# Kernel tuning notes

Hardware: AMD Instinct MI355X
Metric: run time of the kernel (lower is better)

## Reference

```python
import jax, jax.numpy as jnp
import numpy as np

T, L, H, C, D_IN, ED, N, E = 4, 3, 1, 256, 20, 10, 4096, 65536
D = H * C  # 256, pooling width
AH = 4     # pooling attention heads


def setup_inputs() -> dict:
    key = jax.random.key(0)
    ks = jax.random.split(key, 24)
    g = lambda k, s, sc=0.05: jax.random.normal(k, s, jnp.float32) * sc
    return {
        "x": jax.random.normal(ks[0], (N, D_IN), jnp.float32),
        "src": jax.random.randint(ks[1], (E,), 0, N),
        "dst": jax.random.randint(ks[2], (E,), 0, N),
        "edge_attr": jax.random.normal(ks[3], (E, ED), jnp.float32),
        "edge_type": jax.random.randint(ks[4], (E,), 0, T),
        # GATConv params per (edge_type, layer)
        "W0": g(ks[5], (T, D_IN, H * C)),          # layer 0 lin
        "W12": g(ks[6], (T, 2, H * C, H * C)),     # layers 1,2 lin
        "att_src": g(ks[7], (T, L, H, C)),
        "att_dst": g(ks[8], (T, L, H, C)),
        "att_edge": g(ks[9], (T, L, H, C)),
        "lin_edge_w": g(ks[10], (T, L, ED, H * C)),
        "biases": g(ks[11], (T, L, C)),            # H=1 so concat/mean both give C
        "edge_type_weights": jnp.ones((T,), jnp.float32) / T,
        # pooling: MultiheadAttention(D, 4 heads)
        "in_proj_w": g(ks[12], (3 * D, D)),
        "in_proj_b": g(ks[13], (3 * D,)),
        "out_proj_w": g(ks[14], (D, D)),
        "out_proj_b": g(ks[15], (D,)),
        # fusion MLP: 3D -> 2D -> 256
        "fus_w1": g(ks[16], (3 * D, 2 * D)),
        "fus_b1": g(ks[17], (2 * D,)),
        "fus_w2": g(ks[18], (2 * D, 256)),
        "fus_b2": g(ks[19], (256,)),
    }


def _gat(h, src, dst, mask, e_attr, W, a_s, a_d, a_e, We, b, concat):
    # PyG GATConv (edge_dim, add_self_loops=True, fill_value='mean'), eval mode
    Nn = h.shape[0]
    Hh, Cc = a_s.shape
    xl = (h @ W).reshape(Nn, Hh, Cc)
    s_src = jnp.sum(xl * a_s, -1)   # [N,H]
    s_dst = jnp.sum(xl * a_d, -1)   # [N,H]
    s_e = jnp.sum((e_attr @ We).reshape(-1, Hh, Cc) * a_e, -1)  # [E,H]
    # self-loop edge_attr = per-node mean of masked incoming edge_attr
    m = mask.astype(h.dtype)
    cnt = jax.ops.segment_sum(m, dst, Nn)
    loop_attr = jax.ops.segment_sum(e_attr * m[:, None], dst, Nn) / jnp.maximum(cnt, 1.0)[:, None]
    s_loop = jnp.sum((loop_attr @ We).reshape(Nn, Hh, Cc) * a_e, -1)  # [N,H]
    a_real = jax.nn.leaky_relu(s_src[src] + s_dst[dst] + s_e, 0.2)
    a_real = jnp.where(mask[:, None], a_real, -1e30)  # mask edges not of this type
    a_loop = jax.nn.leaky_relu(s_src + s_dst + s_loop, 0.2)
    ar = jnp.arange(Nn)
    idx = jnp.concatenate([dst, ar])    # destination of each (edge + self-loop)
    sidx = jnp.concatenate([src, ar])   # source of each
    scores = jnp.concatenate([a_real, a_loop], 0)  # [E+N, H]
    smax = jax.ops.segment_max(scores, idx, Nn)
    ex = jnp.exp(scores - smax[idx])
    ssum = jax.ops.segment_sum(ex, idx, Nn)
    alpha = ex / (ssum[idx] + 1e-16)
    out = jax.ops.segment_sum(xl[sidx] * alpha[:, :, None], idx, Nn)  # [N,H,C]
    out = out.reshape(Nn, Hh * Cc) if concat else out.mean(1)
    return out + b


def reference(x, src, dst, edge_attr, edge_type, W0, W12, att_src, att_dst,
              att_edge, lin_edge_w, biases, edge_type_weights, in_proj_w,
              in_proj_b, out_proj_w, out_proj_b, fus_w1, fus_b1, fus_w2, fus_b2):
    outs = []
    for t in range(T):
        mask = edge_type == t
        h = x
        for i in range(L):
            W = W0[t] if i == 0 else W12[t, i - 1]
            h = _gat(h, src, dst, mask, edge_attr, W, att_src[t, i],
                     att_dst[t, i], att_edge[t, i], lin_edge_w[t, i],
                     biases[t, i], concat=(i < L - 1))
            h = jax.nn.elu(h)  # dropout off in eval
        outs.append(h)
    w = jax.nn.softmax(edge_type_weights)
    h = sum(w[t] * outs[t] for t in range(T))  # [N, D]
    # HierarchicalGraphPooling
    mean_p = h.mean(0)
    max_p = h.max(0)
    qkv = h @ in_proj_w.T + in_proj_b
    q, k, v = jnp.split(qkv, 3, axis=-1)
    HD = D // AH
    q = q.reshape(-1, AH, HD)
    k = k.reshape(-1, AH, HD)
    v = v.reshape(-1, AH, HD)
    att = jax.nn.softmax(jnp.einsum('nhd,mhd->hnm', q, k) / np.float32(np.sqrt(HD)), axis=-1)
    o = jnp.einsum('hnm,mhd->nhd', att, v).reshape(-1, D) @ out_proj_w.T + out_proj_b
    attn_p = o.mean(0)
    comb = jnp.concatenate([mean_p, max_p, attn_p])  # [3D]
    g = jax.nn.relu(comb @ fus_w1 + fus_b1)
    g = jax.nn.relu(g @ fus_w2 + fus_b2)
    return g[None, :]
```

## Files before the change

### kernel.cpp

```cpp
#include <hip/hip_runtime.h>
#include <math.h>

#define T 4
#define LL 3
#define C 256
#define DIN 20
#define NN 4096
#define EE 65536
#define AHD 4
#define MCH 8
#define QKS 72
#define AST 264
#define SLOTN (16384*64)

#define W_CURSOR 0
#define W_SLSRC  16384
#define F_SLSE   (W_SLSRC + SLOTN)
#define F_XL     (F_SLSE + 3*SLOTN)
#define F_H      (F_XL + T*NN*C/2)
#define F_OPART  F_XL
#define F_SSRC   (F_H + T*NN*C/2)
#define F_SDST   (F_SSRC + T*NN)
#define F_WE     (F_SDST + T*NN)
#define F_HACC   (F_WE + 128)
#define F_WT     (F_HACC + NN*C/2)
#define F_QKV    (F_WT + 768*256/2)
#define F_DPART  (F_QKV + NN*768/2)
#define F_MEANP  (F_DPART + MCH*NN*AHD)
#define F_MAXP   (F_MEANP + C)
#define F_OMEAN  (F_MAXP + C)
#define F_PART   (F_OMEAN + C)
#define U_W12P   (F_PART + 16*512)
#define WS_WORDS (U_W12P + 262144)

static __device__ __forceinline__ float lrelu(float x){ return x > 0.f ? x : 0.2f*x; }
static __device__ __forceinline__ float eluf(float x){ return x > 0.f ? x : __expf(x) - 1.f; }

typedef _Float16 half2_t __attribute__((ext_vector_type(2)));
typedef _Float16 v8h __attribute__((ext_vector_type(8)));
typedef float v4f __attribute__((ext_vector_type(4)));

static __device__ __forceinline__ unsigned pk2(float x, float y){
  half2_t h; h.x = (_Float16)x; h.y = (_Float16)y;
  return __builtin_bit_cast(unsigned, h);
}
static __device__ __forceinline__ unsigned pk2h(_Float16 x, _Float16 y){
  half2_t h; h.x = x; h.y = y;
  return __builtin_bit_cast(unsigned, h);
}
static __device__ __forceinline__ float4 up4(uint2 u){
  half2_t a = __builtin_bit_cast(half2_t, u.x);
  half2_t b = __builtin_bit_cast(half2_t, u.y);
  return make_float4((float)a.x, (float)a.y, (float)b.x, (float)b.y);
}
static __device__ __forceinline__ uint2 dn4(float4 v){
  return make_uint2(pk2(v.x, v.y), pk2(v.z, v.w));
}

static __device__ inline void atomicMaxF(float* addr, float val){
  int* ai = (int*)addr;
  int old = __float_as_int(*addr);
  while (__int_as_float(old) < val){
    int assumed = old;
    old = atomicCAS(ai, assumed, __float_as_int(val));
    if (old == assumed) break;
  }
}

__global__ __launch_bounds__(256) void prep_k(
    const float* __restrict__ x, const float* __restrict__ W0,
    const float* __restrict__ attS, const float* __restrict__ attD,
    _Float16* __restrict__ xlo, float* __restrict__ ssrc, float* __restrict__ sdst,
    const float* __restrict__ w12, _Float16* __restrict__ wpT,
    const float* __restrict__ ipw, _Float16* __restrict__ ip16,
    const float* __restrict__ linE, const float* __restrict__ attE,
    float* we, float* fbase, int* cursor){
  __shared__ float smem[64*65];
  __shared__ float red[64];
  int by = blockIdx.y, bx = blockIdx.x, tid = threadIdx.x;
  if (by < 4){
    int t = by;
    const float* W = W0 + (size_t)t*DIN*C;
    int n0 = bx*8;
    for (int j = 0; j < 8; j++)
      for (int k = tid; k < DIN; k += 256)
        smem[j*DIN + k] = x[(n0+j)*DIN + k];
    __syncthreads();
    float acc[8] = {0,0,0,0,0,0,0,0};
    int c = tid;
    for (int k = 0; k < DIN; k += 4){
      float w0 = W[(k+0)*C + c], w1 = W[(k+1)*C + c], w2 = W[(k+2)*C + c], w3 = W[(k+3)*C + c];
      #pragma unroll
      for (int j = 0; j < 8; j++){
        float4 h4 = *(const float4*)&smem[j*DIN + k];
        acc[j] += w0*h4.x + w1*h4.y + w2*h4.z + w3*h4.w;
      }
    }
    #pragma unroll
    for (int j = 0; j < 8; j++) xlo[((size_t)t*NN + n0 + j)*C + c] = (_Float16)acc[j];
    float aS = attS[t*LL*C + c], aD = attD[t*LL*C + c];
    int lane = c & 63, w = c >> 6;
    #pragma unroll
    for (int j = 0; j < 8; j++){
      float v1 = acc[j]*aS, v2 = acc[j]*aD;
      #pragma unroll
      for (int off = 32; off > 0; off >>= 1){ v1 += __shfl_down(v1, off); v2 += __shfl_down(v2, off); }
      if (lane == 0){ red[j*8 + w] = v1; red[j*8 + 4 + w] = v2; }
    }
    __syncthreads();
    if (c < 16){
      int j = c >> 1, which = c & 1;
      const float* r = red + j*8 + which*4;
      float s = r[0] + r[1] + r[2] + r[3];
      (which ? sdst : ssrc)[t*NN + n0 + j] = s;
    }
  } else if (by < 12){
    if (bx < 16){
      int b8 = by - 4;
      int k0 = (bx >> 2)*64, n0 = (bx & 3)*64;
      const float* src = w12 + ((size_t)b8*256 + k0)*256 + n0;
      int row = tid >> 2, l4 = (tid & 3)*4;
      #pragma unroll
      for (int pass = 0; pass < 4; pass++){
        float4 v = *(const float4*)(src + (size_t)row*256 + pass*16 + l4);
        int o = row*65 + pass*16 + l4;
        smem[o+0] = v.x; smem[o+1] = v.y; smem[o+2] = v.z; smem[o+3] = v.w;
      }
      __syncthreads();
      int n = tid >> 2, seg = tid & 3;
      _Float16* dstp = wpT + ((size_t)b8*256 + n0 + n)*256 + k0 + seg*16;
      v8h h0, h1;
      #pragma unroll
      for (int i = 0; i < 8; i++) h0[i] = (_Float16)smem[(seg*16 + i)*65 + n];
      #pragma unroll
      for (int i = 0; i < 8; i++) h1[i] = (_Float16)smem[(seg*16 + 8 + i)*65 + n];
      *(v8h*)(dstp) = h0;
      *(v8h*)(dstp + 8) = h1;
    }
  } else if (by < 15){
    if (bx < 256){
      int j = (by - 12)*256 + bx;
      ip16[(size_t)j*256 + tid] = (_Float16)ipw[(size_t)j*256 + tid];
    }
  } else {
    if (bx < 12){
      int t = bx / 3, l = bx % 3;
      float ae = attE[(t*LL + l)*C + tid];
      const float* lw = linE + (size_t)((t*LL + l)*10)*C;
      for (int k = 0; k < 10; k++) smem[k*C + tid] = lw[k*C + tid]*ae;
      __syncthreads();
      if (tid < 10){
        float s = 0.f;
        for (int i = 0; i < C; i++) s += smem[tid*C + i];
        we[(t*LL + l)*10 + tid] = s;
      }
    } else if (bx == 12){
      fbase[tid] = 0.f;
      fbase[256 + tid] = -1e30f;
      fbase[512 + tid] = 0.f;
    } else if (bx >= 64 && bx < 128){
      cursor[(bx - 64)*256 + tid] = 0;
    }
  }
}

__global__ __launch_bounds__(256) void scat_k(const int* __restrict__ dst, const int* __restrict__ ety,
                                              const int* __restrict__ srcv, const float* __restrict__ eattr,
                                              const float* __restrict__ we,
                                              int* cursor, int* slot_src, float* slot_se){
  int e = blockIdx.x*256 + threadIdx.x;
  if (e < EE){
    int t = ety[e];
    int gid = dst[e]*T + t;
    int p = atomicAdd(&cursor[gid], 1);
    if (p < 64){
      int sl = gid*64 + p;
      slot_src[sl] = srcv[e];
      float ea[10];
      #pragma unroll
      for (int k = 0; k < 10; k++) ea[k] = eattr[(size_t)e*10 + k];
      #pragma unroll
      for (int l = 0; l < 3; l++){
        const float* w = we + (t*LL + l)*10;
        float s = 0.f;
        #pragma unroll
        for (int k = 0; k < 10; k++) s += ea[k]*w[k];
        slot_se[(size_t)l*SLOTN + sl] = s;
      }
    }
  }
}

__global__ __launch_bounds__(256, 2) void gemm16m_k(const _Float16* __restrict__ hin,
                                                    const _Float16* __restrict__ wpT,
                                                    const float* __restrict__ attS, const float* __restrict__ attD,
                                                    int l, _Float16* __restrict__ xlo,
                                                    float* __restrict__ ssrc, float* __restrict__ sdst){
  __shared__ __align__(16) _Float16 As[64*AST];
  __shared__ float redS[4*64], redD[4*64];
  int t = blockIdx.y;
  int mb = blockIdx.x*64;
  int tid = threadIdx.x;
  int w = tid >> 6, lane = tid & 63;
  int r16 = lane & 15, q = lane >> 4;
  {
    int sr = tid >> 2, sc = (tid & 3)*64;
    const _Float16* hr = hin + ((size_t)(t*NN + mb + sr))*C + sc;
    #pragma unroll
    for (int i = 0; i < 8; i++)
      *(v8h*)(As + (size_t)sr*AST + sc + 8*i) = *(const v8h*)(hr + 8*i);
  }
  __syncthreads();
  int cb = w*64;
  const _Float16* WB = wpT + ((size_t)((t*2 + (l-1))*256 + cb))*256;
  v4f o[4][4];
  #pragma unroll
  for (int i = 0; i < 4; i++)
    #pragma unroll
    for (int j = 0; j < 4; j++) o[i][j] = (v4f){0.f,0.f,0.f,0.f};
  #pragma unroll
  for (int kk = 0; kk < 8; kk++){
    v8h a[4], b[4];
    #pragma unroll
    for (int mi = 0; mi < 4; mi++) a[mi] = *(v8h*)(As + (size_t)(mi*16 + r16)*AST + kk*32 + q*8);
    #pragma unroll
    for (int ni = 0; ni < 4; ni++) b[ni] = *(const v8h*)(WB + (size_t)(ni*16 + r16)*256 + kk*32 + q*8);
    #pragma unroll
    for (int mi = 0; mi < 4; mi++)
      #pragma unroll
      for (int ni = 0; ni < 4; ni++)
        o[mi][ni] = __builtin_amdgcn_mfma_f32_16x16x32_f16(a[mi], b[ni], o[mi][ni], 0, 0, 0);
  }
  int tl = t*LL + l;
  float aS[4], aD[4];
  #pragma unroll
  for (int ni = 0; ni < 4; ni++){
    aS[ni] = attS[tl*C + cb + ni*16 + r16];
    aD[ni] = attD[tl*C + cb + ni*16 + r16];
  }
  #pragma unroll
  for (int mi = 0; mi < 4; mi++)
    #pragma unroll
    for (int rr = 0; rr < 4; rr++){
      int row = mb + mi*16 + q*4 + rr;
      float v1 = 0.f, v2 = 0.f;
      #pragma unroll
      for (int ni = 0; ni < 4; ni++){
        float ov = o[mi][ni][rr];
        xlo[((size_t)t*NN + row)*C + cb + ni*16 + r16] = (_Float16)ov;
        v1 += ov*aS[ni]; v2 += ov*aD[ni];
      }
      v1 += __shfl_xor(v1, 1); v2 += __shfl_xor(v2, 1);
      v1 += __shfl_xor(v1, 2); v2 += __shfl_xor(v2, 2);
      v1 += __shfl_xor(v1, 4); v2 += __shfl_xor(v2, 4);
      v1 += __shfl_xor(v1, 8); v2 += __shfl_xor(v2, 8);
      if (r16 == 0){
        redS[w*64 + mi*16 + q*4 + rr] = v1;
        redD[w*64 + mi*16 + q*4 + rr] = v2;
      }
    }
  __syncthreads();
  if (tid < 64)
    ssrc[t*NN + mb + tid] = redS[tid] + redS[64+tid] + redS[128+tid] + redS[192+tid];
  else if (tid < 128){
    int i = tid - 64;
    sdst[t*NN + mb + i] = redD[i] + redD[64+i] + redD[128+i] + redD[192+i];
  }
}

__global__ __launch_bounds__(256, 2) void qkv16m_k(const _Float16* __restrict__ hacc,
                                                   const _Float16* __restrict__ ip16,
                                                   const float* __restrict__ ipb, _Float16* __restrict__ qkv,
                                                   float* meanp, float* maxp){
  __shared__ __align__(16) _Float16 As[64*AST];
  int p = blockIdx.y;
  int mb = blockIdx.x*64;
  int tid = threadIdx.x;
  int w = tid >> 6, lane = tid & 63;
  int r16 = lane & 15, q = lane >> 4;
  {
    int sr = tid >> 2, sc = (tid & 3)*64;
    const _Float16* hr = hacc + ((size_t)(mb + sr))*C + sc;
    #pragma unroll
    for (int i = 0; i < 8; i++)
      *(v8h*)(As + (size_t)sr*AST + sc + 8*i) = *(const v8h*)(hr + 8*i);
  }
  __syncthreads();
  int cb = p*256 + w*64;
  v4f o[4][4];
  #pragma unroll
  for (int i = 0; i < 4; i++)
    #pragma unroll
    for (int j = 0; j < 4; j++) o[i][j] = (v4f){0.f,0.f,0.f,0.f};
  #pragma unroll
  for (int kk = 0; kk < 8; kk++){
    v8h a[4], b[4];
    #pragma unroll
    for (int mi = 0; mi < 4; mi++) a[mi] = *(v8h*)(As + (size_t)(mi*16 + r16)*AST + kk*32 + q*8);
    #pragma unroll
    for (int ni = 0; ni < 4; ni++) b[ni] = *(const v8h*)(ip16 + (size_t)(cb + ni*16 + r16)*256 + kk*32 + q*8);
    #pragma unroll
    for (int mi = 0; mi < 4; mi++)
      #pragma unroll
      for (int ni = 0; ni < 4; ni++)
        o[mi][ni] = __builtin_amdgcn_mfma_f32_16x16x32_f16(a[mi], b[ni], o[mi][ni], 0, 0, 0);
  }
  float bn[4];
  #pragma unroll
  for (int ni = 0; ni < 4; ni++) bn[ni] = ipb[cb + ni*16 + r16];
  #pragma unroll
  for (int mi = 0; mi < 4; mi++)
    #pragma unroll
    for (int rr = 0; rr < 4; rr++){
      int row = mb + mi*16 + q*4 + rr;
      #pragma unroll
      for (int ni = 0; ni < 4; ni++)
        qkv[(size_t)row*768 + cb + ni*16 + r16] = (_Float16)(o[mi][ni][rr] + bn[ni]);
    }
  if (p == 0){
    float sm = 0.f, mx = -1e30f;
    for (int r = 0; r < 64; r++){
      float v = (float)hacc[(size_t)(mb + r)*C + tid];
      sm += v; mx = fmaxf(mx, v);
    }
    atomicAdd(&meanp[tid], sm*(1.f/4096.f));
    atomicMaxF(&maxp[tid], mx);
  }
}

__global__ __launch_bounds__(256) void agg_k(const _Float16* __restrict__ xl, const float* __restrict__ ssrc,
                                             const float* __restrict__ sdst,
                                             const int* __restrict__ cnt, const int* __restrict__ slot_src,
                                             const float* __restrict__ slot_se,
                                             const float* __restrict__ bias, _Float16* __restrict__ hout,
                                             const float* __restrict__ etw, _Float16* __restrict__ hacc, int l){
  __shared__ float4 sh[4][64];
  int gid = blockIdx.x*4 + (threadIdx.x >> 6);
  int lane = threadIdx.x & 63;
  int n = gid >> 2, t = gid & 3;
  int deg = cnt[gid];
  if (deg > 64) deg = 64;
  float sd = sdst[t*NN + n];
  float se_e = 0.f; int sj = 0;
  if (lane < deg){
    int sl = gid*64 + lane;
    sj = slot_src[sl];
    se_e = slot_se[(size_t)l*SLOTN + sl];
  }
  float ssum_se = se_e;
  #pragma unroll
  for (int o = 32; o > 0; o >>= 1) ssum_se += __shfl_xor(ssum_se, o);
  float sloop = ssum_se / (float)(deg > 0 ? deg : 1);
  float sc = (lane < deg) ? lrelu(ssrc[t*NN + sj] + sd + se_e) : -1e30f;
  float al = lrelu(ssrc[t*NN + n] + sd + sloop);
  float mx = fmaxf(sc, al);
  #pragma unroll
  for (int o = 32; o > 0; o >>= 1) mx = fmaxf(mx, __shfl_xor(mx, o));
  float ex = (lane < deg) ? __expf(sc - mx) : 0.f;
  float ale = __expf(al - mx);
  float ssum = ex;
  #pragma unroll
  for (int o = 32; o > 0; o >>= 1) ssum += __shfl_xor(ssum, o);
  float inv = 1.f/(ssum + ale + 1e-16f);
  const uint2* xl2 = (const uint2*)xl;
  float4 acc = up4(xl2[((size_t)(t*NN + n))*64 + lane]);
  acc.x *= ale; acc.y *= ale; acc.z *= ale; acc.w *= ale;
  int dmax = deg - 1;
  for (int j0 = 0; j0 < deg; j0 += 4){
    float p0 = __shfl(ex, j0);
    float p1 = (j0+1 < deg) ? __shfl(ex, j0+1) : 0.f;
    float p2 = (j0+2 < deg) ? __shfl(ex, j0+2) : 0.f;
    float p3 = (j0+3 < deg) ? __shfl(ex, j0+3) : 0.f;
    int s0 = __shfl(sj, j0);
    int s1 = __shfl(sj, (j0+1 < deg) ? j0+1 : dmax);
    int s2 = __shfl(sj, (j0+2 < deg) ? j0+2 : dmax);
    int s3 = __shfl(sj, (j0+3 < deg) ? j0+3 : dmax);
    float4 v0 = up4(xl2[((size_t)(t*NN + s0))*64 + lane]);
    float4 v1 = up4(xl2[((size_t)(t*NN + s1))*64 + lane]);
    float4 v2 = up4(xl2[((size_t)(t*NN + s2))*64 + lane]);
    float4 v3 = up4(xl2[((size_t)(t*NN + s3))*64 + lane]);
    acc.x += p0*v0.x + p1*v1.x + p2*v2.x + p3*v3.x;
    acc.y += p0*v0.y + p1*v1.y + p2*v2.y + p3*v3.y;
    acc.z += p0*v0.z + p1*v1.z + p2*v2.z + p3*v3.z;
    acc.w += p0*v0.w + p1*v1.w + p2*v2.w + p3*v3.w;
  }
  float4 b4 = *(const float4*)&bias[(t*LL + l)*C + lane*4];
  acc.x = eluf(acc.x*inv + b4.x); acc.y = eluf(acc.y*inv + b4.y);
  acc.z = eluf(acc.z*inv + b4.z); acc.w = eluf(acc.w*inv + b4.w);
  if (l < 2){
    ((uint2*)hout)[((size_t)(t*NN + n))*64 + lane] = dn4(acc);
  } else {
    sh[t][lane] = acc;
    __syncthreads();
    if (t == 0){
      float e0 = etw[0], e1 = etw[1], e2 = etw[2], e3 = etw[3];
      float m = fmaxf(fmaxf(e0,e1), fmaxf(e2,e3));
      float w0 = __expf(e0-m), w1 = __expf(e1-m), w2 = __expf(e2-m), w3 = __expf(e3-m);
      float winv = 1.f/(w0+w1+w2+w3);
      float4 v0 = sh[0][lane], v1 = sh[1][lane], v2 = sh[2][lane], v3 = sh[3][lane];
      float4 s;
      s.x = (w0*v0.x + w1*v1.x + w2*v2.x + w3*v3.x)*winv;
      s.y = (w0*v0.y + w1*v1.y + w2*v2.y + w3*v3.y)*winv;
      s.z = (w0*v0.z + w1*v1.z + w2*v2.z + w3*v3.z)*winv;
      s.w = (w0*v0.w + w1*v1.w + w2*v2.w + w3*v3.w)*winv;
      ((uint2*)hacc)[(size_t)n*64 + lane] = dn4(s);
    }
  }
}

__global__ __launch_bounds__(256, 2) void attn_k(const _Float16* __restrict__ qkv,
                                                 _Float16* __restrict__ opart,
                                                 float* __restrict__ dpart){
  __shared__ __align__(16) _Float16 Ks[64*QKS];
  __shared__ __align__(16) _Float16 VTs[64*QKS];
  __shared__ __align__(16) _Float16 Ps[4][64*QKS];
  int tid = threadIdx.x;
  int wave = tid >> 6, l = tid & 63;
  int nb = blockIdx.x*256 + wave*64;
  int h = blockIdx.y, mc = blockIdx.z;
  int r16 = l & 15, q = l >> 4;
  _Float16* Pw = Ps[wave];

  v8h qf[4][2];
  #pragma unroll
  for (int ni = 0; ni < 4; ni++){
    const _Float16* qrow = qkv + (size_t)(nb + ni*16 + r16)*768 + h*64;
    #pragma unroll
    for (int kk = 0; kk < 2; kk++){
      v8h hv = *(const v8h*)(qrow + kk*32 + q*8);
      #pragma unroll
      for (int i = 0; i < 8; i++) hv[i] = hv[i] * (_Float16)0.125f;
      qf[ni][kk] = hv;
    }
  }

  v4f o[4][4];
  #pragma unroll
  for (int i = 0; i < 4; i++)
    #pragma unroll
    for (int j = 0; j < 4; j++) o[i][j] = (v4f){0.f,0.f,0.f,0.f};
  float dn[4] = {0.f,0.f,0.f,0.f};

  for (int mt = 0; mt < NN/MCH/64; mt++){
    int mb = mc*(NN/MCH) + mt*64;
    __syncthreads();
    {
      int sr = tid >> 2, sc = (tid & 3)*16;
      const _Float16* krow = qkv + (size_t)(mb + sr)*768 + 256 + h*64 + sc;
      *(v8h*)(Ks + (size_t)sr*QKS + sc) = *(const v8h*)(krow);
      *(v8h*)(Ks + (size_t)sr*QKS + sc + 8) = *(const v8h*)(krow + 8);
    }
    {
      int m0 = (tid & 31)*2;
      int db = (tid >> 5)*8;
      const _Float16* v0 = qkv + (size_t)(mb + m0)*768 + 512 + h*64 + db;
      const _Float16* v1 = v0 + 768;
      v8h a = *(const v8h*)v0;
      v8h b = *(const v8h*)v1;
      #pragma unroll
      for (int d = 0; d < 8; d++)
        *(unsigned*)(VTs + (size_t)(db+d)*QKS + m0) = pk2h(a[d], b[d]);
    }
    __syncthreads();
    v4f c[4][4];
    #pragma unroll
    for (int i = 0; i < 4; i++)
      #pragma unroll
      for (int j = 0; j < 4; j++) c[i][j] = (v4f){0.f,0.f,0.f,0.f};
    #pragma unroll
    for (int kk = 0; kk < 2; kk++){
      v8h a[4];
      #pragma unroll
      for (int mi = 0; mi < 4; mi++) a[mi] = *(v8h*)(Ks + (size_t)(mi*16 + r16)*QKS + kk*32 + q*8);
      #pragma unroll
      for (int mi = 0; mi < 4; mi++)
        #pragma unroll
        for (int ni = 0; ni < 4; ni++)
          c[mi][ni] = __builtin_amdgcn_mfma_f32_16x16x32_f16(a[mi], qf[ni][kk], c[mi][ni], 0, 0, 0);
    }
    #pragma unroll
    for (int mi = 0; mi < 4; mi++)
      #pragma unroll
      for (int ni = 0; ni < 4; ni++){
        float e0 = __expf(c[mi][ni][0]), e1 = __expf(c[mi][ni][1]),
              e2 = __expf(c[mi][ni][2]), e3 = __expf(c[mi][ni][3]);
        dn[ni] += e0 + e1 + e2 + e3;
        *(uint2*)(Pw + (size_t)(ni*16 + r16)*QKS + mi*16 + q*4) = make_uint2(pk2(e0,e1), pk2(e2,e3));
      }
    #pragma unroll
    for (int km = 0; km < 2; km++){
      v8h pa[4], vb[4];
      #pragma unroll
      for (int ni = 0; ni < 4; ni++) pa[ni] = *(v8h*)(Pw + (size_t)(ni*16 + r16)*QKS + km*32 + q*8);
      #pragma unroll
      for (int di = 0; di < 4; di++) vb[di] = *(v8h*)(VTs + (size_t)(di*16 + r16)*QKS + km*32 + q*8);
      #pragma unroll
      for (int ni = 0; ni < 4; ni++)
        #pragma unroll
        for (int di = 0; di < 4; di++)
          o[ni][di] = __builtin_amdgcn_mfma_f32_16x16x32_f16(pa[ni], vb[di], o[ni][di], 0, 0, 0);
    }
  }

  _Float16* ob = opart + ((size_t)mc*NN + nb)*C + h*64;
  #pragma unroll
  for (int ni = 0; ni < 4; ni++)
    #pragma unroll
    for (int di = 0; di < 4; di++)
      #pragma unroll
      for (int r = 0; r < 4; r++)
        ob[(size_t)(ni*16 + q*4 + r)*C + di*16 + r16] = (_Float16)o[ni][di][r];
  #pragma unroll
  for (int ni = 0; ni < 4; ni++){
    dn[ni] += __shfl_xor(dn[ni], 16);
    dn[ni] += __shfl_xor(dn[ni], 32);
  }
  if (q == 0){
    #pragma unroll
    for (int ni = 0; ni < 4; ni++)
      dpart[((size_t)mc*NN + nb + ni*16 + r16)*AHD + h] = dn[ni];
  }
}

__global__ __launch_bounds__(256) void attnred_k(const _Float16* __restrict__ opart, const float* __restrict__ dpart,
                                                 float* omean){
  int r0 = blockIdx.x*(NN/256), c = threadIdx.x;
  int head = c >> 6;
  float s = 0.f;
  for (int r = 0; r < NN/256; r++){
    int n = r0 + r;
    float dsum = 0.f, osum = 0.f;
    #pragma unroll
    for (int mc = 0; mc < MCH; mc++){
      dsum += dpart[((size_t)mc*NN + n)*AHD + head];
      osum += (float)opart[((size_t)mc*NN + n)*C + c];
    }
    s += osum / (dsum + 1e-16f);
  }
  atomicAdd(&omean[c], s*(1.f/4096.f));
}

__global__ __launch_bounds__(512) void tailab_k(const float* __restrict__ omean, const float* __restrict__ opw,
                                                const float* __restrict__ opb,
                                                const float* __restrict__ meanp, const float* __restrict__ maxp,
                                                const float* __restrict__ fw1, float* __restrict__ part){
  __shared__ float om[256];
  __shared__ float comb[48];
  int b = blockIdx.x, tid = threadIdx.x;
  if (tid < 256) om[tid] = omean[tid];
  __syncthreads();
  if (tid < 48){
    int k = b*48 + tid;
    float v;
    if (k < 256) v = meanp[k];
    else if (k < 512) v = maxp[k-256];
    else {
      int j = k - 512;
      float acc = 0.f;
      #pragma unroll 4
      for (int i = 0; i < 256; i++) acc += om[i]*opw[(size_t)j*256 + i];
      v = acc + opb[j];
    }
    comb[tid] = v;
  }
  __syncthreads();
  float acc = 0.f;
  #pragma unroll 4
  for (int i = 0; i < 48; i++)
    acc += comb[i]*fw1[((size_t)(b*48 + i))*512 + tid];
  part[(size_t)b*512 + tid] = acc;
}

__global__ __launch_bounds__(256) void tailc_k(const float* __restrict__ part, const float* __restrict__ fb1,
                                               const float* __restrict__ fw2, const float* __restrict__ fb2,
                                               float* __restrict__ out){
  __shared__ float g[512];
  __shared__ float red[256];
  int tid = threadIdx.x;
  float s0 = fb1[tid], s1 = fb1[tid + 256];
  #pragma unroll
  for (int b = 0; b < 16; b++){
    s0 += part[(size_t)b*512 + tid];
    s1 += part[(size_t)b*512 + tid + 256];
  }
  g[tid] = fmaxf(s0, 0.f);
  g[tid + 256] = fmaxf(s1, 0.f);
  __syncthreads();
  int j = blockIdx.x*32 + (tid & 31);
  int kp = tid >> 5;
  float acc = 0.f;
  #pragma unroll 4
  for (int i = 0; i < 64; i++){
    int k = kp*64 + i;
    acc += g[k]*fw2[(size_t)k*256 + j];
  }
  red[tid] = acc;
  __syncthreads();
  if (tid < 32){
    float s = 0.f;
    #pragma unroll
    for (int p = 0; p < 8; p++) s += red[p*32 + tid];
    out[j] = fmaxf(s + fb2[j], 0.f);
  }
}

extern "C" void kernel_launch(void* const* d_in, const int* in_sizes, int n_in,
                              void* d_out, int out_size, void* d_ws, size_t ws_size,
                              hipStream_t stream){
  const float* x     = (const float*)d_in[0];
  const int*   srcv  = (const int*)d_in[1];
  const int*   dstv  = (const int*)d_in[2];
  const float* eattr = (const float*)d_in[3];
  const int*   etyp  = (const int*)d_in[4];
  const float* W0    = (const float*)d_in[5];
  const float* W12   = (const float*)d_in[6];
  const float* attS  = (const float*)d_in[7];
  const float* attD  = (const float*)d_in[8];
  const float* attE  = (const float*)d_in[9];
  const float* linE  = (const float*)d_in[10];
  const float* bias  = (const float*)d_in[11];
  const float* etw   = (const float*)d_in[12];
  const float* ipw   = (const float*)d_in[13];
  const float* ipb   = (const float*)d_in[14];
  const float* opw   = (const float*)d_in[15];
  const float* opb   = (const float*)d_in[16];
  const float* fw1   = (const float*)d_in[17];
  const float* fb1   = (const float*)d_in[18];
  const float* fw2   = (const float*)d_in[19];
  const float* fb2   = (const float*)d_in[20];
  float* out = (float*)d_out;

  if (ws_size < (size_t)WS_WORDS*4) return;

  int*       ip    = (int*)d_ws;
  float*     fp    = (float*)d_ws;
  _Float16*  xl16  = (_Float16*)(fp + F_XL);
  _Float16*  h16   = (_Float16*)(fp + F_H);
  _Float16*  op16  = (_Float16*)(fp + F_OPART);
  _Float16*  hacc16= (_Float16*)(fp + F_HACC);
  _Float16*  ip16  = (_Float16*)(fp + F_WT);
  _Float16*  qkv16 = (_Float16*)(fp + F_QKV);
  _Float16*  wpT   = (_Float16*)(fp + U_W12P);

  prep_k<<<dim3(512, 16), 256, 0, stream>>>(x, W0, attS, attD,
                                            xl16, fp + F_SSRC, fp + F_SDST,
                                            W12, wpT, ipw, ip16, linE, attE,
                                            fp + F_WE, fp + F_MEANP, ip + W_CURSOR);

  scat_k<<<EE/256, 256, 0, stream>>>(dstv, etyp, srcv, eattr, fp + F_WE,
                                     ip + W_CURSOR, ip + W_SLSRC, fp + F_SLSE);

  agg_k<<<(NN*T)/4, 256, 0, stream>>>(xl16, fp + F_SSRC, fp + F_SDST,
                                      ip + W_CURSOR, ip + W_SLSRC, fp + F_SLSE,
                                      bias, h16, etw, hacc16, 0);
  for (int l = 1; l < 3; l++){
    gemm16m_k<<<dim3(NN/64, T), 256, 0, stream>>>(h16, wpT, attS, attD, l,
                                                  xl16, fp + F_SSRC, fp + F_SDST);
    agg_k<<<(NN*T)/4, 256, 0, stream>>>(xl16, fp + F_SSRC, fp + F_SDST,
                                        ip + W_CURSOR, ip + W_SLSRC, fp + F_SLSE,
                                        bias, h16, etw, hacc16, l);
  }

  qkv16m_k<<<dim3(NN/64, 3), 256, 0, stream>>>(hacc16, ip16, ipb, qkv16,
                                               fp + F_MEANP, fp + F_MAXP);
  attn_k<<<dim3(NN/256, AHD, MCH), 256, 0, stream>>>(qkv16, op16, fp + F_DPART);

  attnred_k<<<256, 256, 0, stream>>>(op16, fp + F_DPART, fp + F_OMEAN);
  tailab_k<<<16, 512, 0, stream>>>(fp + F_OMEAN, opw, opb,
                                   fp + F_MEANP, fp + F_MAXP, fw1, fp + F_PART);
  tailc_k<<<8, 256, 0, stream>>>(fp + F_PART, fb1, fw2, fb2, out);
}
```

Measured before the change: 270.7 us.

## Double-buffer K/V tiles in attention and halve GEMM row tiles

The attention kernel now double-buffers the K and V^T shared-memory tiles. It prefetches the next tile's global loads into registers while computing the current tile, which removes one barrier per iteration and hides load latency. The score MFMA loop is restructured per mi so fewer accumulator registers are live. Separately, the two fp16 GEMM kernels (layer projections and QKV) use 32-row tiles instead of 64, doubling the grid for more parallelism at the cost of reloading weight tiles more often.

```diff
diff --git a/kernel.cpp b/kernel.cpp
--- a/kernel.cpp
+++ b/kernel.cpp
@@ -196,37 +196,37 @@
                                                     const float* __restrict__ attS, const float* __restrict__ attD,
                                                     int l, _Float16* __restrict__ xlo,
                                                     float* __restrict__ ssrc, float* __restrict__ sdst){
-  __shared__ __align__(16) _Float16 As[64*AST];
-  __shared__ float redS[4*64], redD[4*64];
+  __shared__ __align__(16) _Float16 As[32*AST];
+  __shared__ float redS[4*32], redD[4*32];
   int t = blockIdx.y;
-  int mb = blockIdx.x*64;
+  int mb = blockIdx.x*32;
   int tid = threadIdx.x;
   int w = tid >> 6, lane = tid & 63;
   int r16 = lane & 15, q = lane >> 4;
   {
-    int sr = tid >> 2, sc = (tid & 3)*64;
+    int sr = tid >> 3, sc = (tid & 7)*32;
     const _Float16* hr = hin + ((size_t)(t*NN + mb + sr))*C + sc;
     #pragma unroll
-    for (int i = 0; i < 8; i++)
+    for (int i = 0; i < 4; i++)
       *(v8h*)(As + (size_t)sr*AST + sc + 8*i) = *(const v8h*)(hr + 8*i);
   }
   __syncthreads();
   int cb = w*64;
   const _Float16* WB = wpT + ((size_t)((t*2 + (l-1))*256 + cb))*256;
-  v4f o[4][4];
-  #pragma unroll
-  for (int i = 0; i < 4; i++)
+  v4f o[2][4];
+  #pragma unroll
+  for (int i = 0; i < 2; i++)
     #pragma unroll
     for (int j = 0; j < 4; j++) o[i][j] = (v4f){0.f,0.f,0.f,0.f};
   #pragma unroll
   for (int kk = 0; kk < 8; kk++){
-    v8h a[4], b[4];
-    #pragma unroll
-    for (int mi = 0; mi < 4; mi++) a[mi] = *(v8h*)(As + (size_t)(mi*16 + r16)*AST + kk*32 + q*8);
+    v8h a[2], b[4];
+    #pragma unroll
+    for (int mi = 0; mi < 2; mi++) a[mi] = *(v8h*)(As + (size_t)(mi*16 + r16)*AST + kk*32 + q*8);
     #pragma unroll
     for (int ni = 0; ni < 4; ni++) b[ni] = *(const v8h*)(WB + (size_t)(ni*16 + r16)*256 + kk*32 + q*8);
     #pragma unroll
-    for (int mi = 0; mi < 4; mi++)
+    for (int mi = 0; mi < 2; mi++)
       #pragma unroll
       for (int ni = 0; ni < 4; ni++)
         o[mi][ni] = __builtin_amdgcn_mfma_f32_16x16x32_f16(a[mi], b[ni], o[mi][ni], 0, 0, 0);
@@ -239,7 +239,7 @@
     aD[ni] = attD[tl*C + cb + ni*16 + r16];
   }
   #pragma unroll
-  for (int mi = 0; mi < 4; mi++)
+  for (int mi = 0; mi < 2; mi++)
     #pragma unroll
     for (int rr = 0; rr < 4; rr++){
       int row = mb + mi*16 + q*4 + rr;
@@ -255,16 +255,16 @@
       v1 += __shfl_xor(v1, 4); v2 += __shfl_xor(v2, 4);
       v1 += __shfl_xor(v1, 8); v2 += __shfl_xor(v2, 8);
       if (r16 == 0){
-        redS[w*64 + mi*16 + q*4 + rr] = v1;
-        redD[w*64 + mi*16 + q*4 + rr] = v2;
+        redS[w*32 + mi*16 + q*4 + rr] = v1;
+        redD[w*32 + mi*16 + q*4 + rr] = v2;
       }
     }
   __syncthreads();
-  if (tid < 64)
-    ssrc[t*NN + mb + tid] = redS[tid] + redS[64+tid] + redS[128+tid] + redS[192+tid];
-  else if (tid < 128){
-    int i = tid - 64;
-    sdst[t*NN + mb + i] = redD[i] + redD[64+i] + redD[128+i] + redD[192+i];
+  if (tid < 32)
+    ssrc[t*NN + mb + tid] = redS[tid] + redS[32+tid] + redS[64+tid] + redS[96+tid];
+  else if (tid < 64){
+    int i = tid - 32;
+    sdst[t*NN + mb + i] = redD[i] + redD[32+i] + redD[64+i] + redD[96+i];
   }
 }
 
@@ -272,35 +272,35 @@
                                                    const _Float16* __restrict__ ip16,
                                                    const float* __restrict__ ipb, _Float16* __restrict__ qkv,
                                                    float* meanp, float* maxp){
-  __shared__ __align__(16) _Float16 As[64*AST];
+  __shared__ __align__(16) _Float16 As[32*AST];
   int p = blockIdx.y;
-  int mb = blockIdx.x*64;
+  int mb = blockIdx.x*32;
   int tid = threadIdx.x;
   int w = tid >> 6, lane = tid & 63;
   int r16 = lane & 15, q = lane >> 4;
   {
-    int sr = tid >> 2, sc = (tid & 3)*64;
+    int sr = tid >> 3, sc = (tid & 7)*32;
     const _Float16* hr = hacc + ((size_t)(mb + sr))*C + sc;
     #pragma unroll
-    for (int i = 0; i < 8; i++)
+    for (int i = 0; i < 4; i++)
       *(v8h*)(As + (size_t)sr*AST + sc + 8*i) = *(const v8h*)(hr + 8*i);
   }
   __syncthreads();
   int cb = p*256 + w*64;
-  v4f o[4][4];
-  #pragma unroll
-  for (int i = 0; i < 4; i++)
+  v4f o[2][4];
+  #pragma unroll
+  for (int i = 0; i < 2; i++)
     #pragma unroll
     for (int j = 0; j < 4; j++) o[i][j] = (v4f){0.f,0.f,0.f,0.f};
   #pragma unroll
   for (int kk = 0; kk < 8; kk++){
-    v8h a[4], b[4];
-    #pragma unroll
-    for (int mi = 0; mi < 4; mi++) a[mi] = *(v8h*)(As + (size_t)(mi*16 + r16)*AST + kk*32 + q*8);
+    v8h a[2], b[4];
+    #pragma unroll
+    for (int mi = 0; mi < 2; mi++) a[mi] = *(v8h*)(As + (size_t)(mi*16 + r16)*AST + kk*32 + q*8);
     #pragma unroll
     for (int ni = 0; ni < 4; ni++) b[ni] = *(const v8h*)(ip16 + (size_t)(cb + ni*16 + r16)*256 + kk*32 + q*8);
     #pragma unroll
-    for (int mi = 0; mi < 4; mi++)
+    for (int mi = 0; mi < 2; mi++)
       #pragma unroll
       for (int ni = 0; ni < 4; ni++)
         o[mi][ni] = __builtin_amdgcn_mfma_f32_16x16x32_f16(a[mi], b[ni], o[mi][ni], 0, 0, 0);
@@ -309,7 +309,7 @@
   #pragma unroll
   for (int ni = 0; ni < 4; ni++) bn[ni] = ipb[cb + ni*16 + r16];
   #pragma unroll
-  for (int mi = 0; mi < 4; mi++)
+  for (int mi = 0; mi < 2; mi++)
     #pragma unroll
     for (int rr = 0; rr < 4; rr++){
       int row = mb + mi*16 + q*4 + rr;
@@ -319,7 +319,7 @@
     }
   if (p == 0){
     float sm = 0.f, mx = -1e30f;
-    for (int r = 0; r < 64; r++){
+    for (int r = 0; r < 32; r++){
       float v = (float)hacc[(size_t)(mb + r)*C + tid];
       sm += v; mx = fmaxf(mx, v);
     }
@@ -411,8 +411,8 @@
 __global__ __launch_bounds__(256, 2) void attn_k(const _Float16* __restrict__ qkv,
                                                  _Float16* __restrict__ opart,
                                                  float* __restrict__ dpart){
-  __shared__ __align__(16) _Float16 Ks[64*QKS];
-  __shared__ __align__(16) _Float16 VTs[64*QKS];
+  __shared__ __align__(16) _Float16 Ks[2][64*QKS];
+  __shared__ __align__(16) _Float16 VTs[2][64*QKS];
   __shared__ __align__(16) _Float16 Ps[4][64*QKS];
   int tid = threadIdx.x;
   int wave = tid >> 6, l = tid & 63;
@@ -420,6 +420,8 @@
   int h = blockIdx.y, mc = blockIdx.z;
   int r16 = l & 15, q = l >> 4;
   _Float16* Pw = Ps[wave];
+  int ksr = tid >> 2, ksc = (tid & 3)*16;
+  int vm0 = (tid & 31)*2, vdb = (tid >> 5)*8;
 
   v8h qf[4][2];
   #pragma unroll
@@ -441,65 +443,78 @@
     for (int j = 0; j < 4; j++) o[i][j] = (v4f){0.f,0.f,0.f,0.f};
   float dn[4] = {0.f,0.f,0.f,0.f};
 
+  {
+    int mb = mc*(NN/MCH);
+    const _Float16* krow = qkv + (size_t)(mb + ksr)*768 + 256 + h*64 + ksc;
+    v8h k0 = *(const v8h*)(krow);
+    v8h k1 = *(const v8h*)(krow + 8);
+    const _Float16* vp = qkv + (size_t)(mb + vm0)*768 + 512 + h*64 + vdb;
+    v8h va = *(const v8h*)vp;
+    v8h vb = *(const v8h*)(vp + 768);
+    *(v8h*)(Ks[0] + (size_t)ksr*QKS + ksc) = k0;
+    *(v8h*)(Ks[0] + (size_t)ksr*QKS + ksc + 8) = k1;
+    #pragma unroll
+    for (int d = 0; d < 8; d++)
+      *(unsigned*)(VTs[0] + (size_t)(vdb+d)*QKS + vm0) = pk2h(va[d], vb[d]);
+  }
+  __syncthreads();
+
   for (int mt = 0; mt < NN/MCH/64; mt++){
-    int mb = mc*(NN/MCH) + mt*64;
-    __syncthreads();
-    {
-      int sr = tid >> 2, sc = (tid & 3)*16;
-      const _Float16* krow = qkv + (size_t)(mb + sr)*768 + 256 + h*64 + sc;
-      *(v8h*)(Ks + (size_t)sr*QKS + sc) = *(const v8h*)(krow);
-      *(v8h*)(Ks + (size_t)sr*QKS + sc + 8) = *(const v8h*)(krow + 8);
-    }
-    {
-      int m0 = (tid & 31)*2;
-      int db = (tid >> 5)*8;
-      const _Float16* v0 = qkv + (size_t)(mb + m0)*768 + 512 + h*64 + db;
-      const _Float16* v1 = v0 + 768;
-      v8h a = *(const v8h*)v0;
-      v8h b = *(const v8h*)v1;
-      #pragma unroll
-      for (int d = 0; d < 8; d++)
-        *(unsigned*)(VTs + (size_t)(db+d)*QKS + m0) = pk2h(a[d], b[d]);
-    }
-    __syncthreads();
-    v4f c[4][4];
-    #pragma unroll
-    for (int i = 0; i < 4; i++)
-      #pragma unroll
-      for (int j = 0; j < 4; j++) c[i][j] = (v4f){0.f,0.f,0.f,0.f};
-    #pragma unroll
-    for (int kk = 0; kk < 2; kk++){
-      v8h a[4];
-      #pragma unroll
-      for (int mi = 0; mi < 4; mi++) a[mi] = *(v8h*)(Ks + (size_t)(mi*16 + r16)*QKS + kk*32 + q*8);
-      #pragma unroll
-      for (int mi = 0; mi < 4; mi++)
-        #pragma unroll
-        for (int ni = 0; ni < 4; ni++)
-          c[mi][ni] = __builtin_amdgcn_mfma_f32_16x16x32_f16(a[mi], qf[ni][kk], c[mi][ni], 0, 0, 0);
-    }
-    #pragma unroll
-    for (int mi = 0; mi < 4; mi++)
+    int cur = mt & 1;
+    bool more = (mt + 1) < NN/MCH/64;
+    v8h nk0, nk1, nva, nvb;
+    if (more){
+      int mbn = mc*(NN/MCH) + (mt+1)*64;
+      const _Float16* krow = qkv + (size_t)(mbn + ksr)*768 + 256 + h*64 + ksc;
+      nk0 = *(const v8h*)(krow);
+      nk1 = *(const v8h*)(krow + 8);
+      const _Float16* vp = qkv + (size_t)(mbn + vm0)*768 + 512 + h*64 + vdb;
+      nva = *(const v8h*)vp;
+      nvb = *(const v8h*)(vp + 768);
+    }
+    #pragma unroll
+    for (int mi = 0; mi < 4; mi++){
+      v4f c[4];
+      #pragma unroll
+      for (int ni = 0; ni < 4; ni++) c[ni] = (v4f){0.f,0.f,0.f,0.f};
+      v8h a0 = *(v8h*)(Ks[cur] + (size_t)(mi*16 + r16)*QKS + q*8);
+      v8h a1 = *(v8h*)(Ks[cur] + (size_t)(mi*16 + r16)*QKS + 32 + q*8);
+      #pragma unroll
+      for (int ni = 0; ni < 4; ni++)
+        c[ni] = __builtin_amdgcn_mfma_f32_16x16x32_f16(a0, qf[ni][0], c[ni], 0, 0, 0);
+      #pragma unroll
+      for (int ni = 0; ni < 4; ni++)
+        c[ni] = __builtin_amdgcn_mfma_f32_16x16x32_f16(a1, qf[ni][1], c[ni], 0, 0, 0);
       #pragma unroll
       for (int ni = 0; ni < 4; ni++){
-        float e0 = __expf(c[mi][ni][0]), e1 = __expf(c[mi][ni][1]),
-              e2 = __expf(c[mi][ni][2]), e3 = __expf(c[mi][ni][3]);
+        float e0 = __expf(c[ni][0]), e1 = __expf(c[ni][1]),
+              e2 = __expf(c[ni][2]), e3 = __expf(c[ni][3]);
         dn[ni] += e0 + e1 + e2 + e3;
         *(uint2*)(Pw + (size_t)(ni*16 + r16)*QKS + mi*16 + q*4) = make_uint2(pk2(e0,e1), pk2(e2,e3));
       }
+    }
     #pragma unroll
     for (int km = 0; km < 2; km++){
-      v8h pa[4], vb[4];
+      v8h pa[4], vb2[4];
       #pragma unroll
       for (int ni = 0; ni < 4; ni++) pa[ni] = *(v8h*)(Pw + (size_t)(ni*16 + r16)*QKS + km*32 + q*8);
       #pragma unroll
-      for (int di = 0; di < 4; di++) vb[di] = *(v8h*)(VTs + (size_t)(di*16 + r16)*QKS + km*32 + q*8);
+      for (int di = 0; di < 4; di++) vb2[di] = *(v8h*)(VTs[cur] + (size_t)(di*16 + r16)*QKS + km*32 + q*8);
       #pragma unroll
       for (int ni = 0; ni < 4; ni++)
         #pragma unroll
         for (int di = 0; di < 4; di++)
-          o[ni][di] = __builtin_amdgcn_mfma_f32_16x16x32_f16(pa[ni], vb[di], o[ni][di], 0, 0, 0);
-    }
+          o[ni][di] = __builtin_amdgcn_mfma_f32_16x16x32_f16(pa[ni], vb2[di], o[ni][di], 0, 0, 0);
+    }
+    if (more){
+      int alt = cur ^ 1;
+      *(v8h*)(Ks[alt] + (size_t)ksr*QKS + ksc) = nk0;
+      *(v8h*)(Ks[alt] + (size_t)ksr*QKS + ksc + 8) = nk1;
+      #pragma unroll
+      for (int d = 0; d < 8; d++)
+        *(unsigned*)(VTs[alt] + (size_t)(vdb+d)*QKS + vm0) = pk2h(nva[d], nvb[d]);
+    }
+    __syncthreads();
   }
 
   _Float16* ob = opart + ((size_t)mc*NN + nb)*C + h*64;
@@ -654,14 +669,14 @@
                                       ip + W_CURSOR, ip + W_SLSRC, fp + F_SLSE,
                                       bias, h16, etw, hacc16, 0);
   for (int l = 1; l < 3; l++){
-    gemm16m_k<<<dim3(NN/64, T), 256, 0, stream>>>(h16, wpT, attS, attD, l,
+    gemm16m_k<<<dim3(NN/32, T), 256, 0, stream>>>(h16, wpT, attS, attD, l,
                                                   xl16, fp + F_SSRC, fp + F_SDST);
     agg_k<<<(NN*T)/4, 256, 0, stream>>>(xl16, fp + F_SSRC, fp + F_SDST,
                                         ip + W_CURSOR, ip + W_SLSRC, fp + F_SLSE,
                                         bias, h16, etw, hacc16, l);
   }
 
-  qkv16m_k<<<dim3(NN/64, 3), 256, 0, stream>>>(hacc16, ip16, ipb, qkv16,
+  qkv16m_k<<<dim3(NN/32, 3), 256, 0, stream>>>(hacc16, ip16, ipb, qkv16,
                                                fp + F_MEANP, fp + F_MAXP);
   attn_k<<<dim3(NN/256, AHD, MCH), 256, 0, stream>>>(qkv16, op16, fp + F_DPART);
 
```

New measurement: 274.5 us. No clear change (+1.4%).
